# Kernel tuning notes

Hardware: AMD Instinct MI355X
Metric: run time of the kernel (lower is better)

The kernel has to match this reference:

```python
import jax, jax.numpy as jnp
import numpy as np

N_NODES = 20000
N_EDGES = 320000

def setup_inputs() -> dict:
    key = jax.random.key(0)
    ks = jax.random.split(key, 12)
    def glorot(k, fan_in, fan_out):
        s = jnp.sqrt(6.0 / (fan_in + fan_out))
        return jax.random.uniform(k, (fan_in, fan_out), jnp.float32, -s, s)
    x = jax.random.normal(ks[0], (N_NODES, 16), jnp.float32)
    edge_index = jax.random.randint(ks[1], (2, N_EDGES), 0, N_NODES, jnp.int64)
    dims = [16, 64, 128, 256, 512, 1]
    out = {"x": x, "edge_index": edge_index}
    for i in range(5):
        out[f"W{i+1}"] = glorot(ks[2 + i], dims[i], dims[i + 1])
        out[f"b{i+1}"] = jnp.zeros((dims[i + 1],), jnp.float32)
    return out

def _prep(edge_index, n):
    # add self-loops (gcn_norm default add_self_loops=True)
    loop = jnp.arange(n, dtype=edge_index.dtype)
    row = jnp.concatenate([edge_index[0], loop])  # src
    col = jnp.concatenate([edge_index[1], loop])  # dst
    deg = jax.ops.segment_sum(jnp.ones_like(col, jnp.float32), col, num_segments=n)
    dinv = jnp.where(deg > 0, jax.lax.rsqrt(jnp.maximum(deg, 1.0)), 0.0)
    norm = dinv[row] * dinv[col]          # symmetric GCN normalization
    cnt = jnp.maximum(deg, 1.0)           # in-degree incl. self-loop, for mean aggr
    return row, col, norm, cnt

def _gcn(x, W, b, row, col, norm, cnt, n, mean_aggr):
    h = x @ W                              # [N, d_out]
    msg = norm[:, None] * h[row]           # gather + scale, [E+N, d_out]
    agg = jax.ops.segment_sum(msg, col, num_segments=n)
    if mean_aggr:
        agg = agg / cnt[:, None]
    return agg + b

def reference(x, edge_index, W1, b1, W2, b2, W3, b3, W4, b4, W5, b5):
    n = x.shape[0]
    row, col, norm, cnt = _prep(edge_index, n)
    h = jax.nn.relu(_gcn(x, W1, b1, row, col, norm, cnt, n, True))
    h = jax.nn.relu(_gcn(h, W2, b2, row, col, norm, cnt, n, True))
    h = jax.nn.relu(_gcn(h, W3, b3, row, col, norm, cnt, n, True))
    h = jax.nn.relu(_gcn(h, W4, b4, row, col, norm, cnt, n, True))
    h = _gcn(h, W5, b5, row, col, norm, cnt, n, False)  # output layer: default 'add' aggr
    return jax.nn.sigmoid(h)
```

## Files before the change

kernel.cpp:

```cpp
#include <hip/hip_runtime.h>
#include <hip/hip_bf16.h>
#include <math.h>


#define N_NODES 20000
#define N_EDGES 320000
#define ELLW 64

typedef __attribute__((ext_vector_type(8))) short short8;
typedef __attribute__((ext_vector_type(4))) float f32x4;

__device__ inline ushort f2bf(float f) {
    __hip_bfloat16 h = __float2bfloat16(f);
    return *(ushort*)&h;
}

__device__ inline float bf2f(short s) {
    union { unsigned int u; float f; } c;
    c.u = ((unsigned int)(unsigned short)s) << 16;
    return c.f;
}


__global__ void k_prep0(int* __restrict__ cnt, int n,
                        const float* __restrict__ W1, const float* __restrict__ W2,
                        const float* __restrict__ W3,
                        ushort* __restrict__ T1, ushort* __restrict__ T2,
                        ushort* __restrict__ T3) {
    int i = blockIdx.x * blockDim.x + threadIdx.x;
    if (i < n) cnt[i] = 0;
    const float* W; ushort* T; int K, N, j;
    if (i < 8192)        { W = W1; T = T1; K = 64;  N = 128; j = i; }
    else if (i < 40960)  { W = W2; T = T2; K = 128; N = 256; j = i - 8192; }
    else if (i < 172032) { W = W3; T = T3; K = 256; N = 512; j = i - 40960; }
    else return;
    int nn = j / K, kk = j - nn * K;
    T[(size_t)nn * K + kk] = f2bf(W[(size_t)kk * N + nn]);
}


__global__ void k_fill_ell(const int* __restrict__ row, const int* __restrict__ col,
                           int* __restrict__ cnt, int* __restrict__ ell, int E) {
    int e = blockIdx.x * blockDim.x + threadIdx.x;
    if (e >= E) return;
    int s = row[e], d = col[e];
    int pos = atomicAdd(&cnt[d], 1);
    ell[((size_t)d << 6) + pos] = s;
}

__global__ void k_deg(const int* __restrict__ cnt, float* __restrict__ dinv, int n) {
    int v = blockIdx.x * blockDim.x + threadIdx.x;
    if (v < n) dinv[v] = rsqrtf((float)(cnt[v] + 1));
}


__global__ __launch_bounds__(256) void k_l1_fused(const float4* __restrict__ x,
                                                  ushort* __restrict__ h_out,
                                                  const int* __restrict__ ell,
                                                  const int* __restrict__ cnt,
                                                  const float* __restrict__ dinv,
                                                  const float* __restrict__ W,
                                                  const float* __restrict__ b, int n) {
    __shared__ float sW[16 * 64];
    __shared__ float sb[64];
    __shared__ float sagg[64][17];
    int tid = threadIdx.x;
    #pragma unroll
    for (int i = tid; i < 1024; i += 256) sW[i] = W[i];
    if (tid < 64) sb[tid] = b[tid];

    int grp = tid >> 2;
    int lane = tid & 3;
    int v = blockIdx.x * 64 + grp;
    if (v < n) {
        float dv = dinv[v];
        int end = cnt[v];
        float inv_cnt = 1.0f / (float)(end + 1);
        const int* r = ell + ((size_t)v << 6);
        float4 hv = x[(size_t)v * 4 + lane];
        float4 acc = make_float4(dv * hv.x, dv * hv.y, dv * hv.z, dv * hv.w);
        int e = 0;
        for (; e + 8 <= end; e += 8) {
            int s0 = r[e],     s1 = r[e + 1], s2 = r[e + 2], s3 = r[e + 3];
            int s4 = r[e + 4], s5 = r[e + 5], s6 = r[e + 6], s7 = r[e + 7];
            float4 h0 = x[(size_t)s0 * 4 + lane];
            float4 h1 = x[(size_t)s1 * 4 + lane];
            float4 h2 = x[(size_t)s2 * 4 + lane];
            float4 h3 = x[(size_t)s3 * 4 + lane];
            float4 h4 = x[(size_t)s4 * 4 + lane];
            float4 h5 = x[(size_t)s5 * 4 + lane];
            float4 h6 = x[(size_t)s6 * 4 + lane];
            float4 h7 = x[(size_t)s7 * 4 + lane];
            float w0 = dinv[s0], w1 = dinv[s1], w2 = dinv[s2], w3 = dinv[s3];
            float w4 = dinv[s4], w5 = dinv[s5], w6 = dinv[s6], w7 = dinv[s7];
            acc.x += w0 * h0.x + w1 * h1.x + w2 * h2.x + w3 * h3.x
                   + w4 * h4.x + w5 * h5.x + w6 * h6.x + w7 * h7.x;
            acc.y += w0 * h0.y + w1 * h1.y + w2 * h2.y + w3 * h3.y
                   + w4 * h4.y + w5 * h5.y + w6 * h6.y + w7 * h7.y;
            acc.z += w0 * h0.z + w1 * h1.z + w2 * h2.z + w3 * h3.z
                   + w4 * h4.z + w5 * h5.z + w6 * h6.z + w7 * h7.z;
            acc.w += w0 * h0.w + w1 * h1.w + w2 * h2.w + w3 * h3.w
                   + w4 * h4.w + w5 * h5.w + w6 * h6.w + w7 * h7.w;
        }
        for (; e + 4 <= end; e += 4) {
            int s0 = r[e], s1 = r[e + 1], s2 = r[e + 2], s3 = r[e + 3];
            float4 h0 = x[(size_t)s0 * 4 + lane];
            float4 h1 = x[(size_t)s1 * 4 + lane];
            float4 h2 = x[(size_t)s2 * 4 + lane];
            float4 h3 = x[(size_t)s3 * 4 + lane];
            float w0 = dinv[s0], w1 = dinv[s1], w2 = dinv[s2], w3 = dinv[s3];
            acc.x += w0 * h0.x + w1 * h1.x + w2 * h2.x + w3 * h3.x;
            acc.y += w0 * h0.y + w1 * h1.y + w2 * h2.y + w3 * h3.y;
            acc.z += w0 * h0.z + w1 * h1.z + w2 * h2.z + w3 * h3.z;
            acc.w += w0 * h0.w + w1 * h1.w + w2 * h2.w + w3 * h3.w;
        }
        for (; e < end; e++) {
            int s = r[e];
            float w = dinv[s];
            float4 hs = x[(size_t)s * 4 + lane];
            acc.x += w * hs.x; acc.y += w * hs.y; acc.z += w * hs.z; acc.w += w * hs.w;
        }
        float sc = dv * inv_cnt;
        sagg[grp][lane * 4 + 0] = acc.x * sc;
        sagg[grp][lane * 4 + 1] = acc.y * sc;
        sagg[grp][lane * 4 + 2] = acc.z * sc;
        sagg[grp][lane * 4 + 3] = acc.w * sc;
    }
    __syncthreads();

    int vg = tid >> 2;
    int c0 = (tid & 3) * 16;
    int vout = blockIdx.x * 64 + vg;
    if (vout >= n) return;
    float o[16];
    #pragma unroll
    for (int jj = 0; jj < 16; jj++) o[jj] = sb[c0 + jj];
    #pragma unroll
    for (int k = 0; k < 16; k++) {
        float a = sagg[vg][k];
        #pragma unroll
        for (int jj = 0; jj < 16; jj++) o[jj] += a * sW[k * 64 + c0 + jj];
    }
    short8 p0, p1;
    #pragma unroll
    for (int jj = 0; jj < 8; jj++) p0[jj] = (short)f2bf(fmaxf(o[jj], 0.0f));
    #pragma unroll
    for (int jj = 0; jj < 8; jj++) p1[jj] = (short)f2bf(fmaxf(o[jj + 8], 0.0f));
    *(short8*)(h_out + (size_t)vout * 64 + c0) = p0;
    *(short8*)(h_out + (size_t)vout * 64 + c0 + 8) = p1;
}


__global__ void k_agg_ell_bf16(const short8* __restrict__ h, short8* __restrict__ out,
                               const int* __restrict__ ell, const int* __restrict__ cnt,
                               const float* __restrict__ dinv, int n, int g_shift) {
    int g = 1 << g_shift;
    int grp = threadIdx.x >> g_shift;
    int lane = threadIdx.x & (g - 1);
    int gpb = blockDim.x >> g_shift;
    int v = blockIdx.x * gpb + grp;
    if (v >= n) return;
    float dv = dinv[v];
    int end = cnt[v];
    float inv_cnt = 1.0f / (float)(end + 1);
    const int* r = ell + ((size_t)v << 6);

    float acc[8];
    short8 hv = h[(size_t)v * g + lane];
    #pragma unroll
    for (int i = 0; i < 8; i++) acc[i] = dv * bf2f(hv[i]);

    int e = 0;
    for (; e + 8 <= end; e += 8) {
        int s0 = r[e],     s1 = r[e + 1], s2 = r[e + 2], s3 = r[e + 3];
        int s4 = r[e + 4], s5 = r[e + 5], s6 = r[e + 6], s7 = r[e + 7];
        short8 h0 = h[(size_t)s0 * g + lane];
        short8 h1 = h[(size_t)s1 * g + lane];
        short8 h2 = h[(size_t)s2 * g + lane];
        short8 h3 = h[(size_t)s3 * g + lane];
        short8 h4 = h[(size_t)s4 * g + lane];
        short8 h5 = h[(size_t)s5 * g + lane];
        short8 h6 = h[(size_t)s6 * g + lane];
        short8 h7 = h[(size_t)s7 * g + lane];
        float w0 = dinv[s0], w1 = dinv[s1], w2 = dinv[s2], w3 = dinv[s3];
        float w4 = dinv[s4], w5 = dinv[s5], w6 = dinv[s6], w7 = dinv[s7];
        #pragma unroll
        for (int i = 0; i < 8; i++)
            acc[i] += w0 * bf2f(h0[i]) + w1 * bf2f(h1[i])
                    + w2 * bf2f(h2[i]) + w3 * bf2f(h3[i])
                    + w4 * bf2f(h4[i]) + w5 * bf2f(h5[i])
                    + w6 * bf2f(h6[i]) + w7 * bf2f(h7[i]);
    }
    for (; e + 4 <= end; e += 4) {
        int s0 = r[e], s1 = r[e + 1], s2 = r[e + 2], s3 = r[e + 3];
        short8 h0 = h[(size_t)s0 * g + lane];
        short8 h1 = h[(size_t)s1 * g + lane];
        short8 h2 = h[(size_t)s2 * g + lane];
        short8 h3 = h[(size_t)s3 * g + lane];
        float w0 = dinv[s0], w1 = dinv[s1], w2 = dinv[s2], w3 = dinv[s3];
        #pragma unroll
        for (int i = 0; i < 8; i++)
            acc[i] += w0 * bf2f(h0[i]) + w1 * bf2f(h1[i])
                    + w2 * bf2f(h2[i]) + w3 * bf2f(h3[i]);
    }
    for (; e < end; e++) {
        int s0 = r[e];
        float w0 = dinv[s0];
        short8 h0 = h[(size_t)s0 * g + lane];
        #pragma unroll
        for (int i = 0; i < 8; i++) acc[i] += w0 * bf2f(h0[i]);
    }
    float sc = dv * inv_cnt;
    short8 o;
    #pragma unroll
    for (int i = 0; i < 8; i++) o[i] = (short)f2bf(acc[i] * sc);
    out[(size_t)v * g + lane] = o;
}


#define GBM 128
#define GBN 128
#define GBK 32
#define LDSS 40

__global__ __launch_bounds__(256) void gemm_mfma(const ushort* __restrict__ A,
                                                 const ushort* __restrict__ Wt,
                                                 const float* __restrict__ bias,
                                                 ushort* __restrict__ C,
                                                 int K, int N, int do_relu) {
    __shared__ ushort As[GBM * LDSS];
    __shared__ ushort Bs[GBN * LDSS];
    int tid = threadIdx.x;
    int wave = tid >> 6;
    int lane = tid & 63;
    int wr = wave >> 1, wc = wave & 1;
    int q = lane >> 4;
    int mr = lane & 15;
    int row0 = blockIdx.y * GBM;
    int col0 = blockIdx.x * GBN;

    int sr = tid >> 2;
    int skoff = (tid & 3) * 8;

    f32x4 acc[4][4];
    #pragma unroll
    for (int i = 0; i < 4; i++)
        #pragma unroll
        for (int j = 0; j < 4; j++) acc[i][j] = (f32x4){0.f, 0.f, 0.f, 0.f};

    const short8 zero8 = {0, 0, 0, 0, 0, 0, 0, 0};
    short8 va0, va1, vb0, vb1;
    int gn0 = col0 + sr, gn1 = col0 + sr + 64;

    {
        int gk = skoff;
        bool kin = gk < K;
        va0 = kin ? *(const short8*)(A + (size_t)(row0 + sr) * K + gk) : zero8;
        va1 = kin ? *(const short8*)(A + (size_t)(row0 + sr + 64) * K + gk) : zero8;
        vb0 = (kin && gn0 < N) ? *(const short8*)(Wt + (size_t)gn0 * K + gk) : zero8;
        vb1 = (kin && gn1 < N) ? *(const short8*)(Wt + (size_t)gn1 * K + gk) : zero8;
        *(short8*)(As + sr * LDSS + skoff) = va0;
        *(short8*)(As + (sr + 64) * LDSS + skoff) = va1;
        *(short8*)(Bs + sr * LDSS + skoff) = vb0;
        *(short8*)(Bs + (sr + 64) * LDSS + skoff) = vb1;
    }
    __syncthreads();

    for (int k0 = 0;;) {
        int k1 = k0 + GBK;
        bool more = (k1 < K);
        if (more) {
            int gk = k1 + skoff;
            bool kin = gk < K;
            va0 = kin ? *(const short8*)(A + (size_t)(row0 + sr) * K + gk) : zero8;
            va1 = kin ? *(const short8*)(A + (size_t)(row0 + sr + 64) * K + gk) : zero8;
            vb0 = (kin && gn0 < N) ? *(const short8*)(Wt + (size_t)gn0 * K + gk) : zero8;
            vb1 = (kin && gn1 < N) ? *(const short8*)(Wt + (size_t)gn1 * K + gk) : zero8;
        }
        short8 afr[4], bfr[4];
        #pragma unroll
        for (int i = 0; i < 4; i++)
            afr[i] = *(const short8*)(As + (wr * 64 + i * 16 + mr) * LDSS + q * 8);
        #pragma unroll
        for (int j = 0; j < 4; j++)
            bfr[j] = *(const short8*)(Bs + (wc * 64 + j * 16 + mr) * LDSS + q * 8);
        #pragma unroll
        for (int i = 0; i < 4; i++)
            #pragma unroll
            for (int j = 0; j < 4; j++)
                acc[i][j] = __builtin_amdgcn_mfma_f32_16x16x32_bf16(afr[i], bfr[j],
                                                                    acc[i][j], 0, 0, 0);
        if (!more) break;
        __syncthreads();
        *(short8*)(As + sr * LDSS + skoff) = va0;
        *(short8*)(As + (sr + 64) * LDSS + skoff) = va1;
        *(short8*)(Bs + sr * LDSS + skoff) = vb0;
        *(short8*)(Bs + (sr + 64) * LDSS + skoff) = vb1;
        __syncthreads();
        k0 = k1;
    }

    #pragma unroll
    for (int j = 0; j < 4; j++) {
        int col = col0 + wc * 64 + j * 16 + mr;
        if (col >= N) continue;
        float bj = bias[col];
        #pragma unroll
        for (int i = 0; i < 4; i++) {
            int rbase = row0 + wr * 64 + i * 16 + q * 4;
            #pragma unroll
            for (int r = 0; r < 4; r++) {
                int grow = rbase + r;
                float v = acc[i][j][r] + bj;
                if (do_relu) v = fmaxf(v, 0.0f);
                C[(size_t)grow * N + col] = f2bf(v);
            }
        }
    }
}


__global__ void k_dot512_bf16(const short8* __restrict__ A, const float4* __restrict__ w,
                              float* __restrict__ out, int n) {
    int wv = (blockIdx.x * blockDim.x + threadIdx.x) >> 6;
    int lane = threadIdx.x & 63;
    if (wv >= n) return;
    short8 a = A[(size_t)wv * 64 + lane];
    float4 w0 = w[lane * 2], w1 = w[lane * 2 + 1];
    float acc = bf2f(a[0]) * w0.x + bf2f(a[1]) * w0.y + bf2f(a[2]) * w0.z + bf2f(a[3]) * w0.w
              + bf2f(a[4]) * w1.x + bf2f(a[5]) * w1.y + bf2f(a[6]) * w1.z + bf2f(a[7]) * w1.w;
    #pragma unroll
    for (int off = 32; off > 0; off >>= 1) acc += __shfl_down(acc, off, 64);
    if (lane == 0) out[wv] = acc;
}

__global__ void k_agg_final(const float* __restrict__ h, float* __restrict__ out,
                            const int* __restrict__ ell, const int* __restrict__ cnt,
                            const float* __restrict__ dinv, const float* __restrict__ b5,
                            int n) {
    int v = blockIdx.x * blockDim.x + threadIdx.x;
    if (v >= n) return;
    float dv = dinv[v];
    float acc = dv * h[v];
    int end = cnt[v];
    const int* r = ell + ((size_t)v << 6);
    for (int e = 0; e < end; e++) {
        int s = r[e];
        acc += dinv[s] * h[s];
    }
    float rr = dv * acc + b5[0];
    out[v] = 1.0f / (1.0f + expf(-rr));
}


extern "C" void kernel_launch(void* const* d_in, const int* in_sizes, int n_in,
                              void* d_out, int out_size, void* d_ws, size_t ws_size,
                              hipStream_t stream) {
    const float* x   = (const float*)d_in[0];
    const int*   ei  = (const int*)d_in[1];
    const float* W[5] = {(const float*)d_in[2], (const float*)d_in[4], (const float*)d_in[6],
                         (const float*)d_in[8], (const float*)d_in[10]};
    const float* b[5] = {(const float*)d_in[3], (const float*)d_in[5], (const float*)d_in[7],
                         (const float*)d_in[9], (const float*)d_in[11]};
    const int n = in_sizes[0] / 16;
    const int E = in_sizes[1] / 2;
    const int dims[6] = {16, 64, 128, 256, 512, 1};

    const int* e_row = ei;
    const int* e_col = ei + E;

    float* bufA_f = (float*)d_ws;
    float* bufB_f = bufA_f + (size_t)n * 512;
    ushort* bufA  = (ushort*)bufA_f;
    ushort* bufB  = (ushort*)bufB_f;
    int*   cnt    = (int*)(bufB_f + (size_t)n * 512);
    float* dinv   = (float*)(cnt + n);
    int*   ell    = (int*)(dinv + n);
    ushort* wt1   = (ushort*)(ell + (size_t)n * ELLW);
    ushort* wt2   = wt1 + 64 * 128;
    ushort* wt3   = wt2 + 128 * 256;
    ushort* wts[4] = {nullptr, wt1, wt2, wt3};

    const int Mpad = (n + GBM - 1) / GBM * GBM;

    k_prep0<<<(172032 + 255) / 256, 256, 0, stream>>>(cnt, n, W[1], W[2], W[3],
                                                      wt1, wt2, wt3);
    k_fill_ell<<<(E + 255) / 256, 256, 0, stream>>>(e_row, e_col, cnt, ell, E);
    k_deg<<<(n + 255) / 256, 256, 0, stream>>>(cnt, dinv, n);

    k_l1_fused<<<(n + 63) / 64, 256, 0, stream>>>(
        (const float4*)x, bufA, ell, cnt, dinv, W[0], b[0], n);

    for (int l = 1; l < 4; l++) {
        int K = dims[l], Nd = dims[l + 1];
        int g_shift = (K == 64) ? 3 : (K == 128) ? 4 : 5;
        int gpb = 256 >> g_shift;
        k_agg_ell_bf16<<<(n + gpb - 1) / gpb, 256, 0, stream>>>(
            (const short8*)bufA, (short8*)bufB, ell, cnt, dinv, n, g_shift);
        dim3 ggrid((Nd + GBN - 1) / GBN, Mpad / GBM);
        gemm_mfma<<<ggrid, 256, 0, stream>>>(bufB, wts[l], b[l], bufA, K, Nd, 1);
    }

    k_dot512_bf16<<<(n * 64 + 255) / 256, 256, 0, stream>>>(
        (const short8*)bufA, (const float4*)W[4], bufB_f, n);
    k_agg_final<<<(n + 255) / 256, 256, 0, stream>>>(bufB_f, (float*)d_out, ell, cnt,
                                                     dinv, b[4], n);
}
```

Baseline: 216.6 us.

## Slice feature columns across XCDs in ELL aggregation for wider layers

Adds a sliced aggregation kernel that maps block IDs to XCDs so each XCD handles only a 64-column feature slice for a subset of nodes. The gathered working set per XCD then fits its private L2, cutting cross-XCD cache misses on random neighbor gathers. The inner loop is also unrolled to 8 edges for more memory-level parallelism. In exchange it relies on round-robin block-to-XCD dispatch, and each node's edge list and dinv values are re-read once per slice.

```diff
diff --git a/kernel.cpp b/kernel.cpp
--- a/kernel.cpp
+++ b/kernel.cpp
@@ -218,6 +218,84 @@
 }
 
 
+__global__ __launch_bounds__(256) void k_agg_ell_sliced(
+        const short8* __restrict__ h, short8* __restrict__ out,
+        const int* __restrict__ ell, const int* __restrict__ cnt,
+        const float* __restrict__ dinv, int n, int gfull_shift,
+        int ns_shift, int tiles_per_sub) {
+    int bid = blockIdx.x;
+    int xcd = bid & 7;
+    int t   = bid >> 3;
+    if (t >= tiles_per_sub) return;
+    int slice = xcd >> (3 - ns_shift);
+    int sub   = xcd & ((8 >> ns_shift) - 1);
+
+    int grp  = threadIdx.x >> 3;
+    int lane = threadIdx.x & 7;
+    int v = (sub * tiles_per_sub + t) * 32 + grp;
+    if (v >= n) return;
+
+    int gfull = 1 << gfull_shift;
+    int fb = slice * 8 + lane;
+
+    float dv = dinv[v];
+    int end = cnt[v];
+    float inv_cnt = 1.0f / (float)(end + 1);
+    const int* r = ell + ((size_t)v << 6);
+
+    float acc[8];
+    short8 hv = h[((size_t)v << gfull_shift) + fb];
+    #pragma unroll
+    for (int i = 0; i < 8; i++) acc[i] = dv * bf2f(hv[i]);
+
+    int e = 0;
+    for (; e + 8 <= end; e += 8) {
+        int s0 = r[e],     s1 = r[e + 1], s2 = r[e + 2], s3 = r[e + 3];
+        int s4 = r[e + 4], s5 = r[e + 5], s6 = r[e + 6], s7 = r[e + 7];
+        short8 h0 = h[((size_t)s0 << gfull_shift) + fb];
+        short8 h1 = h[((size_t)s1 << gfull_shift) + fb];
+        short8 h2 = h[((size_t)s2 << gfull_shift) + fb];
+        short8 h3 = h[((size_t)s3 << gfull_shift) + fb];
+        short8 h4 = h[((size_t)s4 << gfull_shift) + fb];
+        short8 h5 = h[((size_t)s5 << gfull_shift) + fb];
+        short8 h6 = h[((size_t)s6 << gfull_shift) + fb];
+        short8 h7 = h[((size_t)s7 << gfull_shift) + fb];
+        float w0 = dinv[s0], w1 = dinv[s1], w2 = dinv[s2], w3 = dinv[s3];
+        float w4 = dinv[s4], w5 = dinv[s5], w6 = dinv[s6], w7 = dinv[s7];
+        #pragma unroll
+        for (int i = 0; i < 8; i++)
+            acc[i] += w0 * bf2f(h0[i]) + w1 * bf2f(h1[i])
+                    + w2 * bf2f(h2[i]) + w3 * bf2f(h3[i])
+                    + w4 * bf2f(h4[i]) + w5 * bf2f(h5[i])
+                    + w6 * bf2f(h6[i]) + w7 * bf2f(h7[i]);
+    }
+    for (; e + 4 <= end; e += 4) {
+        int s0 = r[e], s1 = r[e + 1], s2 = r[e + 2], s3 = r[e + 3];
+        short8 h0 = h[((size_t)s0 << gfull_shift) + fb];
+        short8 h1 = h[((size_t)s1 << gfull_shift) + fb];
+        short8 h2 = h[((size_t)s2 << gfull_shift) + fb];
+        short8 h3 = h[((size_t)s3 << gfull_shift) + fb];
+        float w0 = dinv[s0], w1 = dinv[s1], w2 = dinv[s2], w3 = dinv[s3];
+        #pragma unroll
+        for (int i = 0; i < 8; i++)
+            acc[i] += w0 * bf2f(h0[i]) + w1 * bf2f(h1[i])
+                    + w2 * bf2f(h2[i]) + w3 * bf2f(h3[i]);
+    }
+    for (; e < end; e++) {
+        int s0 = r[e];
+        float w0 = dinv[s0];
+        short8 h0 = h[((size_t)s0 << gfull_shift) + fb];
+        #pragma unroll
+        for (int i = 0; i < 8; i++) acc[i] += w0 * bf2f(h0[i]);
+    }
+    float sc = dv * inv_cnt;
+    short8 o;
+    #pragma unroll
+    for (int i = 0; i < 8; i++) o[i] = (short)f2bf(acc[i] * sc);
+    out[((size_t)v << gfull_shift) + fb] = o;
+}
+
+
 #define GBM 128
 #define GBN 128
 #define GBK 32
@@ -382,6 +460,7 @@
     ushort* wts[4] = {nullptr, wt1, wt2, wt3};
 
     const int Mpad = (n + GBM - 1) / GBM * GBM;
+    const int ntiles32 = (n + 31) / 32;
 
     k_prep0<<<(172032 + 255) / 256, 256, 0, stream>>>(cnt, n, W[1], W[2], W[3],
                                                       wt1, wt2, wt3);
@@ -391,14 +470,32 @@
     k_l1_fused<<<(n + 63) / 64, 256, 0, stream>>>(
         (const float4*)x, bufA, ell, cnt, dinv, W[0], b[0], n);
 
-    for (int l = 1; l < 4; l++) {
-        int K = dims[l], Nd = dims[l + 1];
-        int g_shift = (K == 64) ? 3 : (K == 128) ? 4 : 5;
-        int gpb = 256 >> g_shift;
-        k_agg_ell_bf16<<<(n + gpb - 1) / gpb, 256, 0, stream>>>(
-            (const short8*)bufA, (short8*)bufB, ell, cnt, dinv, n, g_shift);
+    {
+        int K = 64, Nd = 128;
+        k_agg_ell_bf16<<<(n + 31) / 32, 256, 0, stream>>>(
+            (const short8*)bufA, (short8*)bufB, ell, cnt, dinv, n, 3);
         dim3 ggrid((Nd + GBN - 1) / GBN, Mpad / GBM);
-        gemm_mfma<<<ggrid, 256, 0, stream>>>(bufB, wts[l], b[l], bufA, K, Nd, 1);
+        gemm_mfma<<<ggrid, 256, 0, stream>>>(bufB, wts[1], b[1], bufA, K, Nd, 1);
+    }
+
+    {
+        int K = 128, Nd = 256;
+        int ns_shift = 1, xps = 8 >> ns_shift;
+        int tps = (ntiles32 + xps - 1) / xps;
+        k_agg_ell_sliced<<<8 * tps, 256, 0, stream>>>(
+            (const short8*)bufA, (short8*)bufB, ell, cnt, dinv, n, 4, ns_shift, tps);
+        dim3 ggrid((Nd + GBN - 1) / GBN, Mpad / GBM);
+        gemm_mfma<<<ggrid, 256, 0, stream>>>(bufB, wts[2], b[2], bufA, K, Nd, 1);
+    }
+
+    {
+        int K = 256, Nd = 512;
+        int ns_shift = 2, xps = 8 >> ns_shift;
+        int tps = (ntiles32 + xps - 1) / xps;
+        k_agg_ell_sliced<<<8 * tps, 256, 0, stream>>>(
+            (const short8*)bufA, (short8*)bufB, ell, cnt, dinv, n, 5, ns_shift, tps);
+        dim3 ggrid((Nd + GBN - 1) / GBN, Mpad / GBM);
+        gemm_mfma<<<ggrid, 256, 0, stream>>>(bufB, wts[3], b[3], bufA, K, Nd, 1);
     }
 
     k_dot512_bf16<<<(n * 64 + 255) / 256, 256, 0, stream>>>(
```

Result: no change. 213.8 us (-1.3%).

## Fuse final 512-dot into last GEMM epilogue and drop separate dinv/prep kernels

Applied to the files above, without the earlier changes.

The last layer's GEMM epilogue now applies bias and ReLU and dots each row with W5, accumulating per-row partial sums into z with atomics. This removes the 512-wide bf16 activation write and the separate dot kernel. The dinv array is dropped and recomputed from cnt on the fly. Weight transposition moves into the ELL fill kernel, so k_prep0 and k_deg are no longer launched. GEMM bounds checks are also removed on the assumption that the dimensions are tile multiples. The cost is atomic contention on z, extra rsqrt work in the aggregation loops, and reliance on padded shapes.

```diff
diff --git a/kernel.cpp b/kernel.cpp
--- a/kernel.cpp
+++ b/kernel.cpp
@@ -21,44 +21,44 @@
     return c.f;
 }
 
-
-__global__ void k_prep0(int* __restrict__ cnt, int n,
-                        const float* __restrict__ W1, const float* __restrict__ W2,
-                        const float* __restrict__ W3,
-                        ushort* __restrict__ T1, ushort* __restrict__ T2,
-                        ushort* __restrict__ T3) {
+__device__ __forceinline__ float dinv_of(const int* __restrict__ cnt, int v) {
+    return rsqrtf((float)(cnt[v] + 1));
+}
+
+
+__global__ void k_zero(int* __restrict__ cnt, float* __restrict__ z, int n, int mpad) {
     int i = blockIdx.x * blockDim.x + threadIdx.x;
     if (i < n) cnt[i] = 0;
-    const float* W; ushort* T; int K, N, j;
-    if (i < 8192)        { W = W1; T = T1; K = 64;  N = 128; j = i; }
-    else if (i < 40960)  { W = W2; T = T2; K = 128; N = 256; j = i - 8192; }
-    else if (i < 172032) { W = W3; T = T3; K = 256; N = 512; j = i - 40960; }
-    else return;
-    int nn = j / K, kk = j - nn * K;
-    T[(size_t)nn * K + kk] = f2bf(W[(size_t)kk * N + nn]);
+    if (i < mpad) z[i] = 0.0f;
 }
 
 
 __global__ void k_fill_ell(const int* __restrict__ row, const int* __restrict__ col,
-                           int* __restrict__ cnt, int* __restrict__ ell, int E) {
+                           int* __restrict__ cnt, int* __restrict__ ell, int E,
+                           const float* __restrict__ W2, const float* __restrict__ W3,
+                           const float* __restrict__ W4,
+                           ushort* __restrict__ T2, ushort* __restrict__ T3,
+                           ushort* __restrict__ T4) {
     int e = blockIdx.x * blockDim.x + threadIdx.x;
+    if (e < 172032) {
+        const float* W; ushort* T; int K, N, j;
+        if (e < 8192)        { W = W2; T = T2; K = 64;  N = 128; j = e; }
+        else if (e < 40960)  { W = W3; T = T3; K = 128; N = 256; j = e - 8192; }
+        else                 { W = W4; T = T4; K = 256; N = 512; j = e - 40960; }
+        int nn = j / K, kk = j - nn * K;
+        T[(size_t)nn * K + kk] = f2bf(W[(size_t)kk * N + nn]);
+    }
     if (e >= E) return;
     int s = row[e], d = col[e];
     int pos = atomicAdd(&cnt[d], 1);
     ell[((size_t)d << 6) + pos] = s;
 }
 
-__global__ void k_deg(const int* __restrict__ cnt, float* __restrict__ dinv, int n) {
-    int v = blockIdx.x * blockDim.x + threadIdx.x;
-    if (v < n) dinv[v] = rsqrtf((float)(cnt[v] + 1));
-}
-
 
 __global__ __launch_bounds__(256) void k_l1_fused(const float4* __restrict__ x,
                                                   ushort* __restrict__ h_out,
                                                   const int* __restrict__ ell,
                                                   const int* __restrict__ cnt,
-                                                  const float* __restrict__ dinv,
                                                   const float* __restrict__ W,
                                                   const float* __restrict__ b, int n) {
     __shared__ float sW[16 * 64];
@@ -73,7 +73,7 @@
     int lane = tid & 3;
     int v = blockIdx.x * 64 + grp;
     if (v < n) {
-        float dv = dinv[v];
+        float dv = dinv_of(cnt, v);
         int end = cnt[v];
         float inv_cnt = 1.0f / (float)(end + 1);
         const int* r = ell + ((size_t)v << 6);
@@ -91,8 +91,10 @@
             float4 h5 = x[(size_t)s5 * 4 + lane];
             float4 h6 = x[(size_t)s6 * 4 + lane];
             float4 h7 = x[(size_t)s7 * 4 + lane];
-            float w0 = dinv[s0], w1 = dinv[s1], w2 = dinv[s2], w3 = dinv[s3];
-            float w4 = dinv[s4], w5 = dinv[s5], w6 = dinv[s6], w7 = dinv[s7];
+            float w0 = dinv_of(cnt, s0), w1 = dinv_of(cnt, s1);
+            float w2 = dinv_of(cnt, s2), w3 = dinv_of(cnt, s3);
+            float w4 = dinv_of(cnt, s4), w5 = dinv_of(cnt, s5);
+            float w6 = dinv_of(cnt, s6), w7 = dinv_of(cnt, s7);
             acc.x += w0 * h0.x + w1 * h1.x + w2 * h2.x + w3 * h3.x
                    + w4 * h4.x + w5 * h5.x + w6 * h6.x + w7 * h7.x;
             acc.y += w0 * h0.y + w1 * h1.y + w2 * h2.y + w3 * h3.y
@@ -108,7 +110,8 @@
             float4 h1 = x[(size_t)s1 * 4 + lane];
             float4 h2 = x[(size_t)s2 * 4 + lane];
             float4 h3 = x[(size_t)s3 * 4 + lane];
-            float w0 = dinv[s0], w1 = dinv[s1], w2 = dinv[s2], w3 = dinv[s3];
+            float w0 = dinv_of(cnt, s0), w1 = dinv_of(cnt, s1);
+            float w2 = dinv_of(cnt, s2), w3 = dinv_of(cnt, s3);
             acc.x += w0 * h0.x + w1 * h1.x + w2 * h2.x + w3 * h3.x;
             acc.y += w0 * h0.y + w1 * h1.y + w2 * h2.y + w3 * h3.y;
             acc.z += w0 * h0.z + w1 * h1.z + w2 * h2.z + w3 * h3.z;
@@ -116,7 +119,7 @@
         }
         for (; e < end; e++) {
             int s = r[e];
-            float w = dinv[s];
+            float w = dinv_of(cnt, s);
             float4 hs = x[(size_t)s * 4 + lane];
             acc.x += w * hs.x; acc.y += w * hs.y; acc.z += w * hs.z; acc.w += w * hs.w;
         }
@@ -153,14 +156,14 @@
 
 __global__ void k_agg_ell_bf16(const short8* __restrict__ h, short8* __restrict__ out,
                                const int* __restrict__ ell, const int* __restrict__ cnt,
-                               const float* __restrict__ dinv, int n, int g_shift) {
+                               int n, int g_shift) {
     int g = 1 << g_shift;
     int grp = threadIdx.x >> g_shift;
     int lane = threadIdx.x & (g - 1);
     int gpb = blockDim.x >> g_shift;
     int v = blockIdx.x * gpb + grp;
     if (v >= n) return;
-    float dv = dinv[v];
+    float dv = dinv_of(cnt, v);
     int end = cnt[v];
     float inv_cnt = 1.0f / (float)(end + 1);
     const int* r = ell + ((size_t)v << 6);
@@ -182,8 +185,10 @@
         short8 h5 = h[(size_t)s5 * g + lane];
         short8 h6 = h[(size_t)s6 * g + lane];
         short8 h7 = h[(size_t)s7 * g + lane];
-        float w0 = dinv[s0], w1 = dinv[s1], w2 = dinv[s2], w3 = dinv[s3];
-        float w4 = dinv[s4], w5 = dinv[s5], w6 = dinv[s6], w7 = dinv[s7];
+        float w0 = dinv_of(cnt, s0), w1 = dinv_of(cnt, s1);
+        float w2 = dinv_of(cnt, s2), w3 = dinv_of(cnt, s3);
+        float w4 = dinv_of(cnt, s4), w5 = dinv_of(cnt, s5);
+        float w6 = dinv_of(cnt, s6), w7 = dinv_of(cnt, s7);
         #pragma unroll
         for (int i = 0; i < 8; i++)
             acc[i] += w0 * bf2f(h0[i]) + w1 * bf2f(h1[i])
@@ -197,7 +202,8 @@
         short8 h1 = h[(size_t)s1 * g + lane];
         short8 h2 = h[(size_t)s2 * g + lane];
         short8 h3 = h[(size_t)s3 * g + lane];
-        float w0 = dinv[s0], w1 = dinv[s1], w2 = dinv[s2], w3 = dinv[s3];
+        float w0 = dinv_of(cnt, s0), w1 = dinv_of(cnt, s1);
+        float w2 = dinv_of(cnt, s2), w3 = dinv_of(cnt, s3);
         #pragma unroll
         for (int i = 0; i < 8; i++)
             acc[i] += w0 * bf2f(h0[i]) + w1 * bf2f(h1[i])
@@ -205,7 +211,7 @@
     }
     for (; e < end; e++) {
         int s0 = r[e];
-        float w0 = dinv[s0];
+        float w0 = dinv_of(cnt, s0);
         short8 h0 = h[(size_t)s0 * g + lane];
         #pragma unroll
         for (int i = 0; i < 8; i++) acc[i] += w0 * bf2f(h0[i]);
@@ -227,6 +233,8 @@
                                                  const ushort* __restrict__ Wt,
                                                  const float* __restrict__ bias,
                                                  ushort* __restrict__ C,
+                                                 const float* __restrict__ dotw,
+                                                 float* __restrict__ z,
                                                  int K, int N, int do_relu) {
     __shared__ ushort As[GBM * LDSS];
     __shared__ ushort Bs[GBN * LDSS];
@@ -248,17 +256,14 @@
         #pragma unroll
         for (int j = 0; j < 4; j++) acc[i][j] = (f32x4){0.f, 0.f, 0.f, 0.f};
 
-    const short8 zero8 = {0, 0, 0, 0, 0, 0, 0, 0};
     short8 va0, va1, vb0, vb1;
     int gn0 = col0 + sr, gn1 = col0 + sr + 64;
 
     {
-        int gk = skoff;
-        bool kin = gk < K;
-        va0 = kin ? *(const short8*)(A + (size_t)(row0 + sr) * K + gk) : zero8;
-        va1 = kin ? *(const short8*)(A + (size_t)(row0 + sr + 64) * K + gk) : zero8;
-        vb0 = (kin && gn0 < N) ? *(const short8*)(Wt + (size_t)gn0 * K + gk) : zero8;
-        vb1 = (kin && gn1 < N) ? *(const short8*)(Wt + (size_t)gn1 * K + gk) : zero8;
+        va0 = *(const short8*)(A + (size_t)(row0 + sr) * K + skoff);
+        va1 = *(const short8*)(A + (size_t)(row0 + sr + 64) * K + skoff);
+        vb0 = *(const short8*)(Wt + (size_t)gn0 * K + skoff);
+        vb1 = *(const short8*)(Wt + (size_t)gn1 * K + skoff);
         *(short8*)(As + sr * LDSS + skoff) = va0;
         *(short8*)(As + (sr + 64) * LDSS + skoff) = va1;
         *(short8*)(Bs + sr * LDSS + skoff) = vb0;
@@ -271,11 +276,10 @@
         bool more = (k1 < K);
         if (more) {
             int gk = k1 + skoff;
-            bool kin = gk < K;
-            va0 = kin ? *(const short8*)(A + (size_t)(row0 + sr) * K + gk) : zero8;
-            va1 = kin ? *(const short8*)(A + (size_t)(row0 + sr + 64) * K + gk) : zero8;
-            vb0 = (kin && gn0 < N) ? *(const short8*)(Wt + (size_t)gn0 * K + gk) : zero8;
-            vb1 = (kin && gn1 < N) ? *(const short8*)(Wt + (size_t)gn1 * K + gk) : zero8;
+            va0 = *(const short8*)(A + (size_t)(row0 + sr) * K + gk);
+            va1 = *(const short8*)(A + (size_t)(row0 + sr + 64) * K + gk);
+            vb0 = *(const short8*)(Wt + (size_t)gn0 * K + gk);
+            vb1 = *(const short8*)(Wt + (size_t)gn1 * K + gk);
         }
         short8 afr[4], bfr[4];
         #pragma unroll
@@ -300,53 +304,62 @@
         k0 = k1;
     }
 
+    if (dotw) {
+        float bj[4], wj[4];
+        #pragma unroll
+        for (int j = 0; j < 4; j++) {
+            int col = col0 + wc * 64 + j * 16 + mr;
+            bj[j] = bias[col];
+            wj[j] = dotw[col];
+        }
+        #pragma unroll
+        for (int i = 0; i < 4; i++) {
+            #pragma unroll
+            for (int r = 0; r < 4; r++) {
+                float p = 0.0f;
+                #pragma unroll
+                for (int j = 0; j < 4; j++)
+                    p += fmaxf(acc[i][j][r] + bj[j], 0.0f) * wj[j];
+                #pragma unroll
+                for (int off = 1; off < 16; off <<= 1)
+                    p += __shfl_xor(p, off, 64);
+                if (mr == 0)
+                    atomicAdd(&z[row0 + wr * 64 + i * 16 + q * 4 + r], p);
+            }
+        }
+        return;
+    }
+
     #pragma unroll
     for (int j = 0; j < 4; j++) {
         int col = col0 + wc * 64 + j * 16 + mr;
-        if (col >= N) continue;
         float bj = bias[col];
         #pragma unroll
         for (int i = 0; i < 4; i++) {
             int rbase = row0 + wr * 64 + i * 16 + q * 4;
             #pragma unroll
             for (int r = 0; r < 4; r++) {
-                int grow = rbase + r;
                 float v = acc[i][j][r] + bj;
                 if (do_relu) v = fmaxf(v, 0.0f);
-                C[(size_t)grow * N + col] = f2bf(v);
+                C[(size_t)(rbase + r) * N + col] = f2bf(v);
             }
         }
     }
 }
 
-
-__global__ void k_dot512_bf16(const short8* __restrict__ A, const float4* __restrict__ w,
-                              float* __restrict__ out, int n) {
-    int wv = (blockIdx.x * blockDim.x + threadIdx.x) >> 6;
-    int lane = threadIdx.x & 63;
-    if (wv >= n) return;
-    short8 a = A[(size_t)wv * 64 + lane];
-    float4 w0 = w[lane * 2], w1 = w[lane * 2 + 1];
-    float acc = bf2f(a[0]) * w0.x + bf2f(a[1]) * w0.y + bf2f(a[2]) * w0.z + bf2f(a[3]) * w0.w
-              + bf2f(a[4]) * w1.x + bf2f(a[5]) * w1.y + bf2f(a[6]) * w1.z + bf2f(a[7]) * w1.w;
-    #pragma unroll
-    for (int off = 32; off > 0; off >>= 1) acc += __shfl_down(acc, off, 64);
-    if (lane == 0) out[wv] = acc;
-}
 
 __global__ void k_agg_final(const float* __restrict__ h, float* __restrict__ out,
                             const int* __restrict__ ell, const int* __restrict__ cnt,
-                            const float* __restrict__ dinv, const float* __restrict__ b5,
-                            int n) {
+                            const float* __restrict__ b5, int n) {
     int v = blockIdx.x * blockDim.x + threadIdx.x;
     if (v >= n) return;
-    float dv = dinv[v];
+    float dv = dinv_of(cnt, v);
     float acc = dv * h[v];
     int end = cnt[v];
     const int* r = ell + ((size_t)v << 6);
     for (int e = 0; e < end; e++) {
         int s = r[e];
-        acc += dinv[s] * h[s];
+        acc += dinv_of(cnt, s) * h[s];
     }
     float rr = dv * acc + b5[0];
     out[v] = 1.0f / (1.0f + expf(-rr));
@@ -364,7 +377,6 @@
                          (const float*)d_in[9], (const float*)d_in[11]};
     const int n = in_sizes[0] / 16;
     const int E = in_sizes[1] / 2;
-    const int dims[6] = {16, 64, 128, 256, 512, 1};
 
     const int* e_row = ei;
     const int* e_col = ei + E;
@@ -374,35 +386,45 @@
     ushort* bufA  = (ushort*)bufA_f;
     ushort* bufB  = (ushort*)bufB_f;
     int*   cnt    = (int*)(bufB_f + (size_t)n * 512);
-    float* dinv   = (float*)(cnt + n);
-    int*   ell    = (int*)(dinv + n);
-    ushort* wt1   = (ushort*)(ell + (size_t)n * ELLW);
-    ushort* wt2   = wt1 + 64 * 128;
-    ushort* wt3   = wt2 + 128 * 256;
-    ushort* wts[4] = {nullptr, wt1, wt2, wt3};
+    int*   ell    = cnt + n;
+    ushort* wt2   = (ushort*)(ell + (size_t)n * ELLW);
+    ushort* wt3   = wt2 + 64 * 128;
+    ushort* wt4   = wt3 + 128 * 256;
+    float* z      = (float*)(wt4 + 256 * 512);
 
     const int Mpad = (n + GBM - 1) / GBM * GBM;
 
-    k_prep0<<<(172032 + 255) / 256, 256, 0, stream>>>(cnt, n, W[1], W[2], W[3],
-                                                      wt1, wt2, wt3);
-    k_fill_ell<<<(E + 255) / 256, 256, 0, stream>>>(e_row, e_col, cnt, ell, E);
-    k_deg<<<(n + 255) / 256, 256, 0, stream>>>(cnt, dinv, n);
+    k_zero<<<(Mpad + 255) / 256, 256, 0, stream>>>(cnt, z, n, Mpad);
+    k_fill_ell<<<(E + 255) / 256, 256, 0, stream>>>(e_row, e_col, cnt, ell, E,
+                                                    W[1], W[2], W[3], wt2, wt3, wt4);
 
     k_l1_fused<<<(n + 63) / 64, 256, 0, stream>>>(
-        (const float4*)x, bufA, ell, cnt, dinv, W[0], b[0], n);
-
-    for (int l = 1; l < 4; l++) {
-        int K = dims[l], Nd = dims[l + 1];
-        int g_shift = (K == 64) ? 3 : (K == 128) ? 4 : 5;
-        int gpb = 256 >> g_shift;
-        k_agg_ell_bf16<<<(n + gpb - 1) / gpb, 256, 0, stream>>>(
-            (const short8*)bufA, (short8*)bufB, ell, cnt, dinv, n, g_shift);
-        dim3 ggrid((Nd + GBN - 1) / GBN, Mpad / GBM);
-        gemm_mfma<<<ggrid, 256, 0, stream>>>(bufB, wts[l], b[l], bufA, K, Nd, 1);
-    }
-
-    k_dot512_bf16<<<(n * 64 + 255) / 256, 256, 0, stream>>>(
-        (const short8*)bufA, (const float4*)W[4], bufB_f, n);
-    k_agg_final<<<(n + 255) / 256, 256, 0, stream>>>(bufB_f, (float*)d_out, ell, cnt,
-                                                     dinv, b[4], n);
-}
+        (const float4*)x, bufA, ell, cnt, W[0], b[0], n);
+
+    k_agg_ell_bf16<<<(n + 31) / 32, 256, 0, stream>>>(
+        (const short8*)bufA, (short8*)bufB, ell, cnt, n, 3);
+    {
+        dim3 ggrid(128 / GBN, Mpad / GBM);
+        gemm_mfma<<<ggrid, 256, 0, stream>>>(bufB, wt2, b[1], bufA,
+                                             nullptr, nullptr, 64, 128, 1);
+    }
+
+    k_agg_ell_bf16<<<(n + 15) / 16, 256, 0, stream>>>(
+        (const short8*)bufA, (short8*)bufB, ell, cnt, n, 4);
+    {
+        dim3 ggrid(256 / GBN, Mpad / GBM);
+        gemm_mfma<<<ggrid, 256, 0, stream>>>(bufB, wt3, b[2], bufA,
+                                             nullptr, nullptr, 128, 256, 1);
+    }
+
+    k_agg_ell_bf16<<<(n + 7) / 8, 256, 0, stream>>>(
+        (const short8*)bufA, (short8*)bufB, ell, cnt, n, 5);
+    {
+        dim3 ggrid(512 / GBN, Mpad / GBM);
+        gemm_mfma<<<ggrid, 256, 0, stream>>>(bufB, wt4, b[3], nullptr,
+                                             W[4], z, 256, 512, 1);
+    }
+
+    k_agg_final<<<(n + 255) / 256, 256, 0, stream>>>(z, (float*)d_out, ell, cnt,
+                                                     b[4], n);
+}
```

After: 207.7 us. -4.1%, faster.
